# Performance work log

Hardware: AMD Instinct MI355X
Metric: run time of the kernel (lower is better)

The kernel has to match this reference:

```python
import jax, jax.numpy as jnp
import numpy as np

B, C, H, W = 1, 512, 24, 24
N_HEADS, WS = 8, 7
PAD = WS // 2
HEAD_DIM = C // N_HEADS


def setup_inputs() -> dict:
    key = jax.random.key(0)
    ks = jax.random.split(key, 7)
    s = 0.02
    return {
        "x": jax.random.normal(ks[0], (B, C, H, W), dtype=jnp.float32),
        "Wq": s * jax.random.normal(ks[1], (C, C), dtype=jnp.float32),
        "bq": s * jax.random.normal(ks[2], (C,), dtype=jnp.float32),
        "Wk": s * jax.random.normal(ks[3], (C, C), dtype=jnp.float32),
        "bk": s * jax.random.normal(ks[4], (C,), dtype=jnp.float32),
        "Wv": s * jax.random.normal(ks[5], (C, C), dtype=jnp.float32),
        "bv": s * jax.random.normal(ks[6], (C,), dtype=jnp.float32),
        # module initializes gamma to zero; use small nonzero so output depends on attention
        "gamma": jnp.full((1,), 0.1, dtype=jnp.float32),
    }


def _conv1x1(z, Wt, bt):
    # 1x1 Conv2d == per-pixel GEMM over channels
    return jnp.einsum("bchw,oc->bohw", z, Wt) + bt[None, :, None, None]


def _windows(z):
    # z: (B, C, H+ws-1, W+ws-1) -> (B, n_heads, head_dim, ws*ws*H*W)
    # matches torch unfold(2,ws,1).unfold(3,ws,1).permute(0,1,4,5,2,3).view(...)
    taps = [z[:, :, di:di + H, dj:dj + W] for di in range(WS) for dj in range(WS)]
    w = jnp.stack(taps, axis=2)  # (B, C, ws*ws, H, W)
    return w.reshape(B, N_HEADS, HEAD_DIM, WS * WS * H * W)


def reference(x, Wq, bq, Wk, bk, Wv, bv, gamma):
    q = _conv1x1(x, Wq, bq).reshape(B, N_HEADS, HEAD_DIM, H * W)  # (B,h,d,HW)
    xp = jnp.pad(x, ((0, 0), (0, 0), (PAD, PAD), (PAD, PAD)), mode="reflect")
    k = _windows(_conv1x1(xp, Wk, bk))  # (B,h,d,ws^2*HW)
    v = _windows(_conv1x1(xp, Wv, bv))  # (B,h,d,ws^2*HW)
    # NOTE: as written in the source, each query attends to ALL ws^2*H*W keys
    energy = jnp.einsum("bhdq,bhdk->bhqk", q, k)  # (B,h,HW,ws^2*HW)
    attn = jax.nn.softmax(energy, axis=-1)
    out_w = jnp.einsum("bhqk,bhdk->bhdq", attn, v).reshape(B, C, H, W)
    return gamma * out_w + x
```

## Files before the change

### kernel.cpp

```cpp
#include <hip/hip_runtime.h>

#define HW   576
#define CC   512
#define PW   30
#define PPK  1024

typedef float f32x4 __attribute__((ext_vector_type(4)));
typedef short s16x8 __attribute__((ext_vector_type(8)));

__device__ __forceinline__ unsigned short f2bf(float f) {
    unsigned u = __float_as_uint(f);
    return (unsigned short)((u + 0x7FFFu + ((u >> 16) & 1u)) >> 16);
}
__device__ __forceinline__ float bf2f(unsigned short h) {
    return __uint_as_float((unsigned)h << 16);
}
__device__ __forceinline__ int smapf(int p) {
    if (p >= 900) return 576;
    const int y = p / PW, xw = p - y * PW;
    int iy = y - 3;  iy = (iy < 0) ? -iy : (iy > 23 ? 46 - iy : iy);
    int ix = xw - 3; ix = (ix < 0) ? -ix : (ix > 23 ? 46 - ix : ix);
    return iy * 24 + ix;
}

#define OFF_QT 0u
#define OFF_KT 589824u
#define OFF_VP 1638400u
#define OFF_XT 2686976u
#define OFF_WB 3277824u

__global__ __launch_bounds__(256) void cvtT(
    const float* __restrict__ x,
    const float* __restrict__ Wq, const float* __restrict__ Wk,
    const float* __restrict__ Wv,
    unsigned short* __restrict__ xT, unsigned short* __restrict__ wb)
{
    const int b = blockIdx.x, t = threadIdx.x;
    if (b < 72) {
        __shared__ float tile[64][65];
        const int pt = b % 9, ct = b / 9;
        const int p0 = pt * 64, c0 = ct * 64;
        const int tr = t >> 4, tc4 = (t & 15) * 4;
        #pragma unroll
        for (int cr = 0; cr < 4; ++cr) {
            const int row = cr * 16 + tr;
            const float4 v = *(const float4*)&x[(size_t)(c0 + row) * HW + p0 + tc4];
            tile[row][tc4 + 0] = v.x;
            tile[row][tc4 + 1] = v.y;
            tile[row][tc4 + 2] = v.z;
            tile[row][tc4 + 3] = v.w;
        }
        __syncthreads();
        #pragma unroll
        for (int cr = 0; cr < 4; ++cr) {
            const int prow = cr * 16 + tr;
            ushort4 o;
            o.x = f2bf(tile[tc4 + 0][prow]);
            o.y = f2bf(tile[tc4 + 1][prow]);
            o.z = f2bf(tile[tc4 + 2][prow]);
            o.w = f2bf(tile[tc4 + 3][prow]);
            *(ushort4*)&xT[(size_t)(p0 + prow) * CC + c0 + tc4] = o;
        }
    } else if (b == 72) {
        if (t < 128) *(ushort4*)&xT[(size_t)576 * CC + t * 4] = (ushort4){0, 0, 0, 0};
    } else {
        const int wi = (b - 73) * 2048 + t * 8;
        const int sel = wi >> 18, off = wi & 262143;
        const float* src = (sel == 0) ? Wq : (sel == 1) ? Wk : Wv;
        const float4 v0 = *(const float4*)&src[off];
        const float4 v1 = *(const float4*)&src[off + 4];
        ushort4 o0, o1;
        o0.x = f2bf(v0.x); o0.y = f2bf(v0.y); o0.z = f2bf(v0.z); o0.w = f2bf(v0.w);
        o1.x = f2bf(v1.x); o1.y = f2bf(v1.y); o1.z = f2bf(v1.z); o1.w = f2bf(v1.w);
        *(ushort4*)&wb[wi]     = o0;
        *(ushort4*)&wb[wi + 4] = o1;
    }
}

__global__ __launch_bounds__(256) void qkv_direct(
    const unsigned short* __restrict__ xT, const unsigned short* __restrict__ wb,
    const float* __restrict__ bq, const float* __restrict__ bk,
    const float* __restrict__ bv,
    unsigned short* __restrict__ qT, unsigned short* __restrict__ kT,
    unsigned short* __restrict__ vP)
{
    const int t = threadIdx.x;
    const int w = blockIdx.x * 4 + (t >> 6);
    const int lane = t & 63, fr = lane & 15, u = lane >> 4;

    int sel, m0, n0;
    if (w < 576)       { sel = 0; m0 = (w >> 4) << 4;               n0 = (w & 15) << 5; }
    else if (w < 1600) { const int k = w - 576;  sel = 1; m0 = (k >> 4) << 4; n0 = (k & 15) << 5; }
    else               { const int k = w - 1600; sel = 2; m0 = (k >> 5) << 4; n0 = (k & 31) << 5; }

    const unsigned short *A, *B;
    int ar, bn0, bn1;
    if (sel == 0)      { A = xT;          B = wb;          ar = m0 + fr;
                         bn0 = n0 + fr;          bn1 = n0 + 16 + fr; }
    else if (sel == 1) { A = xT;          B = wb + 262144; ar = smapf(m0 + fr);
                         bn0 = n0 + fr;          bn1 = n0 + 16 + fr; }
    else               { A = wb + 524288; B = xT;          ar = m0 + fr;
                         bn0 = smapf(n0 + fr);   bn1 = smapf(n0 + 16 + fr); }

    const unsigned short* Ap  = A + (size_t)ar  * CC + u * 8;
    const unsigned short* Bp0 = B + (size_t)bn0 * CC + u * 8;
    const unsigned short* Bp1 = B + (size_t)bn1 * CC + u * 8;

    f32x4 acc0 = (f32x4){0.f, 0.f, 0.f, 0.f};
    f32x4 acc1 = (f32x4){0.f, 0.f, 0.f, 0.f};
    #pragma unroll 8
    for (int k0 = 0; k0 < CC; k0 += 32) {
        const s16x8 a  = *(const s16x8*)(Ap  + k0);
        const s16x8 b0 = *(const s16x8*)(Bp0 + k0);
        const s16x8 b1 = *(const s16x8*)(Bp1 + k0);
        acc0 = __builtin_amdgcn_mfma_f32_16x16x32_bf16(a, b0, acc0, 0, 0, 0);
        acc1 = __builtin_amdgcn_mfma_f32_16x16x32_bf16(a, b1, acc1, 0, 0, 0);
    }

    #pragma unroll
    for (int ni = 0; ni < 2; ++ni) {
        const f32x4 acc = ni ? acc1 : acc0;
        #pragma unroll
        for (int r = 0; r < 4; ++r) {
            const int m = m0 + u * 4 + r;
            const int n = n0 + ni * 16 + fr;
            if (sel == 0) {
                qT[((size_t)(n >> 6) * HW + m) * 64 + (n & 63)] = f2bf(acc[r] + bq[n]);
            } else if (sel == 1) {
                kT[((size_t)(n >> 6) * PPK + m) * 64 + (n & 63)] = f2bf(acc[r] + bk[n]);
            } else {
                vP[((size_t)(m >> 6) * 64 + (m & 63)) * PPK + n] = f2bf(acc[r] + bv[m]);
            }
        }
    }
}

#define WLS 1040
__global__ __launch_bounds__(256) void attn4(
    const unsigned short* __restrict__ qT, const unsigned short* __restrict__ kT,
    const unsigned short* __restrict__ vP, const float* __restrict__ x,
    const float* __restrict__ gamma, float* __restrict__ out)
{
    const int q0 = blockIdx.x * 16;
    const int hd = blockIdx.y;
    const int t  = threadIdx.x;
    const int lane = t & 63, w = t >> 6;
    const int fr = lane & 15, u = lane >> 4;

    __shared__ float cnt_s[PPK];
    __shared__ __align__(16) unsigned short Wl[16 * WLS];
    __shared__ float mw[64], lw[64], sca[16];

    for (int i = t; i < PPK; i += 256) {
        float c = 0.f;
        if (i < 900) {
            const int y = i / PW, xw = i - y * PW;
            int cy = y + 1;  if (PW - y  < cy) cy = PW - y;  if (cy > 7) cy = 7;
            int cx = xw + 1; if (PW - xw < cx) cx = PW - xw; if (cx > 7) cx = 7;
            c = (float)(cy * cx);
        }
        cnt_s[i] = c;
    }

    const unsigned short* qrow = qT + ((size_t)hd * HW + q0 + fr) * 64 + u * 8;
    const s16x8 b0 = *(const s16x8*)qrow;
    const s16x8 b1 = *(const s16x8*)(qrow + 32);

    f32x4 e[16];
    #pragma unroll
    for (int t4 = 0; t4 < 16; ++t4) {
        const unsigned short* krow =
            kT + ((size_t)hd * PPK + w * 256 + t4 * 16 + fr) * 64 + u * 8;
        const s16x8 a0 = *(const s16x8*)krow;
        const s16x8 a1 = *(const s16x8*)(krow + 32);
        f32x4 a = (f32x4){0.f, 0.f, 0.f, 0.f};
        a = __builtin_amdgcn_mfma_f32_16x16x32_bf16(a0, b0, a, 0, 0, 0);
        a = __builtin_amdgcn_mfma_f32_16x16x32_bf16(a1, b1, a, 0, 0, 0);
        e[t4] = a;
    }

    float m = -1e30f;
    #pragma unroll
    for (int t4 = 0; t4 < 16; ++t4)
        #pragma unroll
        for (int r = 0; r < 4; ++r) m = fmaxf(m, e[t4][r]);
    m = fmaxf(m, __shfl_xor(m, 16));
    m = fmaxf(m, __shfl_xor(m, 32));
    if (lane < 16) mw[w * 16 + lane] = m;
    __syncthreads();
    const float mq = fmaxf(fmaxf(mw[fr], mw[16 + fr]), fmaxf(mw[32 + fr], mw[48 + fr]));

    float sum = 0.f;
    #pragma unroll
    for (int t4 = 0; t4 < 16; ++t4) {
        const float4 c4 = *(const float4*)&cnt_s[w * 256 + t4 * 16 + u * 4];
        const float cw[4] = {c4.x, c4.y, c4.z, c4.w};
        unsigned short wb4[4];
        #pragma unroll
        for (int r = 0; r < 4; ++r) {
            const float wv2 = cw[r] * __expf(e[t4][r] - mq);
            sum += wv2;
            wb4[r] = f2bf(wv2);
        }
        const int ho = fr * WLS + w * 256 + t4 * 16 + u * 4;
        *(unsigned*)&Wl[ho]     = (unsigned)wb4[0] | ((unsigned)wb4[1] << 16);
        *(unsigned*)&Wl[ho + 2] = (unsigned)wb4[2] | ((unsigned)wb4[3] << 16);
    }
    sum += __shfl_xor(sum, 16);
    sum += __shfl_xor(sum, 32);
    if (lane < 16) lw[w * 16 + lane] = sum;
    __syncthreads();

    if (t < 16) {
        const float lq = lw[t] + lw[16 + t] + lw[32 + t] + lw[48 + t];
        sca[t] = gamma[0] / lq;
    }

    f32x4 o = (f32x4){0.f, 0.f, 0.f, 0.f};
    const unsigned short* vrow =
        vP + ((size_t)hd * 64 + w * 16 + fr) * PPK + u * 8;
    #pragma unroll 8
    for (int c = 0; c < 32; ++c) {
        const s16x8 aw = *(const s16x8*)&Wl[fr * WLS + c * 32 + u * 8];
        const s16x8 bv2 = *(const s16x8*)(vrow + c * 32);
        o = __builtin_amdgcn_mfma_f32_16x16x32_bf16(aw, bv2, o, 0, 0, 0);
    }
    __syncthreads();

    const int d = hd * 64 + w * 16 + fr;
    const size_t gb = (size_t)d * HW + q0 + u * 4;
    const float4 x4 = *(const float4*)&x[gb];
    float4 o4;
    o4.x = fmaf(sca[u * 4 + 0], o[0], x4.x);
    o4.y = fmaf(sca[u * 4 + 1], o[1], x4.y);
    o4.z = fmaf(sca[u * 4 + 2], o[2], x4.z);
    o4.w = fmaf(sca[u * 4 + 3], o[3], x4.w);
    *(float4*)&out[gb] = o4;
}

extern "C" void kernel_launch(void* const* d_in, const int* in_sizes, int n_in,
                              void* d_out, int out_size, void* d_ws, size_t ws_size,
                              hipStream_t stream) {
    const float* x     = (const float*)d_in[0];
    const float* Wq    = (const float*)d_in[1];
    const float* bq    = (const float*)d_in[2];
    const float* Wk    = (const float*)d_in[3];
    const float* bk    = (const float*)d_in[4];
    const float* Wv    = (const float*)d_in[5];
    const float* bv    = (const float*)d_in[6];
    const float* gamma = (const float*)d_in[7];
    float* out = (float*)d_out;

    char* wsb = (char*)d_ws;
    unsigned short* qT = (unsigned short*)(wsb + OFF_QT);
    unsigned short* kT = (unsigned short*)(wsb + OFF_KT);
    unsigned short* vP = (unsigned short*)(wsb + OFF_VP);
    unsigned short* xT = (unsigned short*)(wsb + OFF_XT);
    unsigned short* wb = (unsigned short*)(wsb + OFF_WB);

    cvtT<<<dim3(457), 256, 0, stream>>>(x, Wq, Wk, Wv, xT, wb);
    qkv_direct<<<dim3(656), 256, 0, stream>>>(xT, wb, bq, bk, bv, qT, kT, vP);
    attn4<<<dim3(36, 8), 256, 0, stream>>>(qT, kT, vP, x, gamma, out);
}
```

Baseline: 109.0 us.

## Use 32x32 QKV tiles per wave and split attention across 8 waves

The QKV projection kernel now computes a 32x32 output tile per wave with four MFMA accumulators, so each A and B fragment is loaded once and reused twice, halving the wave count. The attention kernel doubles to 512 threads: each wave scores 128 keys instead of 256, and the PV product is split over two key halves whose partial sums are combined through shared memory. This trades fewer redundant global loads and more parallelism for extra reduction steps and synchronisation.

```diff
diff --git a/kernel.cpp b/kernel.cpp
--- a/kernel.cpp
+++ b/kernel.cpp
@@ -89,54 +89,66 @@
     const int lane = t & 63, fr = lane & 15, u = lane >> 4;
 
     int sel, m0, n0;
-    if (w < 576)       { sel = 0; m0 = (w >> 4) << 4;               n0 = (w & 15) << 5; }
-    else if (w < 1600) { const int k = w - 576;  sel = 1; m0 = (k >> 4) << 4; n0 = (k & 15) << 5; }
-    else               { const int k = w - 1600; sel = 2; m0 = (k >> 5) << 4; n0 = (k & 31) << 5; }
+    if (w < 288)      { sel = 0; m0 = (w >> 4) << 5;               n0 = (w & 15) << 5; }
+    else if (w < 800) { const int k = w - 288; sel = 1; m0 = (k >> 4) << 5; n0 = (k & 15) << 5; }
+    else              { const int k = w - 800; sel = 2; m0 = (k >> 5) << 5; n0 = (k & 31) << 5; }
 
     const unsigned short *A, *B;
-    int ar, bn0, bn1;
-    if (sel == 0)      { A = xT;          B = wb;          ar = m0 + fr;
-                         bn0 = n0 + fr;          bn1 = n0 + 16 + fr; }
-    else if (sel == 1) { A = xT;          B = wb + 262144; ar = smapf(m0 + fr);
-                         bn0 = n0 + fr;          bn1 = n0 + 16 + fr; }
-    else               { A = wb + 524288; B = xT;          ar = m0 + fr;
-                         bn0 = smapf(n0 + fr);   bn1 = smapf(n0 + 16 + fr); }
-
-    const unsigned short* Ap  = A + (size_t)ar  * CC + u * 8;
+    int ar0, ar1, bn0, bn1;
+    if (sel == 0)      { A = xT;          B = wb;
+                         ar0 = m0 + fr;         ar1 = m0 + 16 + fr;
+                         bn0 = n0 + fr;         bn1 = n0 + 16 + fr; }
+    else if (sel == 1) { A = xT;          B = wb + 262144;
+                         ar0 = smapf(m0 + fr);  ar1 = smapf(m0 + 16 + fr);
+                         bn0 = n0 + fr;         bn1 = n0 + 16 + fr; }
+    else               { A = wb + 524288; B = xT;
+                         ar0 = m0 + fr;         ar1 = m0 + 16 + fr;
+                         bn0 = smapf(n0 + fr);  bn1 = smapf(n0 + 16 + fr); }
+
+    const unsigned short* Ap0 = A + (size_t)ar0 * CC + u * 8;
+    const unsigned short* Ap1 = A + (size_t)ar1 * CC + u * 8;
     const unsigned short* Bp0 = B + (size_t)bn0 * CC + u * 8;
     const unsigned short* Bp1 = B + (size_t)bn1 * CC + u * 8;
 
-    f32x4 acc0 = (f32x4){0.f, 0.f, 0.f, 0.f};
-    f32x4 acc1 = (f32x4){0.f, 0.f, 0.f, 0.f};
-    #pragma unroll 8
+    f32x4 acc00 = (f32x4){0.f, 0.f, 0.f, 0.f};
+    f32x4 acc01 = (f32x4){0.f, 0.f, 0.f, 0.f};
+    f32x4 acc10 = (f32x4){0.f, 0.f, 0.f, 0.f};
+    f32x4 acc11 = (f32x4){0.f, 0.f, 0.f, 0.f};
+    #pragma unroll 4
     for (int k0 = 0; k0 < CC; k0 += 32) {
-        const s16x8 a  = *(const s16x8*)(Ap  + k0);
+        const s16x8 a0 = *(const s16x8*)(Ap0 + k0);
+        const s16x8 a1 = *(const s16x8*)(Ap1 + k0);
         const s16x8 b0 = *(const s16x8*)(Bp0 + k0);
         const s16x8 b1 = *(const s16x8*)(Bp1 + k0);
-        acc0 = __builtin_amdgcn_mfma_f32_16x16x32_bf16(a, b0, acc0, 0, 0, 0);
-        acc1 = __builtin_amdgcn_mfma_f32_16x16x32_bf16(a, b1, acc1, 0, 0, 0);
-    }
-
-    #pragma unroll
-    for (int ni = 0; ni < 2; ++ni) {
-        const f32x4 acc = ni ? acc1 : acc0;
-        #pragma unroll
-        for (int r = 0; r < 4; ++r) {
-            const int m = m0 + u * 4 + r;
+        acc00 = __builtin_amdgcn_mfma_f32_16x16x32_bf16(a0, b0, acc00, 0, 0, 0);
+        acc01 = __builtin_amdgcn_mfma_f32_16x16x32_bf16(a0, b1, acc01, 0, 0, 0);
+        acc10 = __builtin_amdgcn_mfma_f32_16x16x32_bf16(a1, b0, acc10, 0, 0, 0);
+        acc11 = __builtin_amdgcn_mfma_f32_16x16x32_bf16(a1, b1, acc11, 0, 0, 0);
+    }
+
+    #pragma unroll
+    for (int mi = 0; mi < 2; ++mi) {
+        #pragma unroll
+        for (int ni = 0; ni < 2; ++ni) {
+            const f32x4 acc = mi ? (ni ? acc11 : acc10) : (ni ? acc01 : acc00);
             const int n = n0 + ni * 16 + fr;
-            if (sel == 0) {
-                qT[((size_t)(n >> 6) * HW + m) * 64 + (n & 63)] = f2bf(acc[r] + bq[n]);
-            } else if (sel == 1) {
-                kT[((size_t)(n >> 6) * PPK + m) * 64 + (n & 63)] = f2bf(acc[r] + bk[n]);
-            } else {
-                vP[((size_t)(m >> 6) * 64 + (m & 63)) * PPK + n] = f2bf(acc[r] + bv[m]);
+            #pragma unroll
+            for (int r = 0; r < 4; ++r) {
+                const int m = m0 + mi * 16 + u * 4 + r;
+                if (sel == 0) {
+                    qT[((size_t)(n >> 6) * HW + m) * 64 + (n & 63)] = f2bf(acc[r] + bq[n]);
+                } else if (sel == 1) {
+                    kT[((size_t)(n >> 6) * PPK + m) * 64 + (n & 63)] = f2bf(acc[r] + bk[n]);
+                } else {
+                    vP[((size_t)(m >> 6) * 64 + (m & 63)) * PPK + n] = f2bf(acc[r] + bv[m]);
+                }
             }
         }
     }
 }
 
 #define WLS 1040
-__global__ __launch_bounds__(256) void attn4(
+__global__ __launch_bounds__(512) void attn5(
     const unsigned short* __restrict__ qT, const unsigned short* __restrict__ kT,
     const unsigned short* __restrict__ vP, const float* __restrict__ x,
     const float* __restrict__ gamma, float* __restrict__ out)
@@ -149,9 +161,10 @@
 
     __shared__ float cnt_s[PPK];
     __shared__ __align__(16) unsigned short Wl[16 * WLS];
-    __shared__ float mw[64], lw[64], sca[16];
-
-    for (int i = t; i < PPK; i += 256) {
+    __shared__ float mw[128], lw[128], sca[16];
+    __shared__ float4 red[4][64];
+
+    for (int i = t; i < PPK; i += 512) {
         float c = 0.f;
         if (i < 900) {
             const int y = i / PW, xw = i - y * PW;
@@ -166,11 +179,11 @@
     const s16x8 b0 = *(const s16x8*)qrow;
     const s16x8 b1 = *(const s16x8*)(qrow + 32);
 
-    f32x4 e[16];
-    #pragma unroll
-    for (int t4 = 0; t4 < 16; ++t4) {
+    f32x4 e[8];
+    #pragma unroll
+    for (int t4 = 0; t4 < 8; ++t4) {
         const unsigned short* krow =
-            kT + ((size_t)hd * PPK + w * 256 + t4 * 16 + fr) * 64 + u * 8;
+            kT + ((size_t)hd * PPK + w * 128 + t4 * 16 + fr) * 64 + u * 8;
         const s16x8 a0 = *(const s16x8*)krow;
         const s16x8 a1 = *(const s16x8*)(krow + 32);
         f32x4 a = (f32x4){0.f, 0.f, 0.f, 0.f};
@@ -181,19 +194,21 @@
 
     float m = -1e30f;
     #pragma unroll
-    for (int t4 = 0; t4 < 16; ++t4)
+    for (int t4 = 0; t4 < 8; ++t4)
         #pragma unroll
         for (int r = 0; r < 4; ++r) m = fmaxf(m, e[t4][r]);
     m = fmaxf(m, __shfl_xor(m, 16));
     m = fmaxf(m, __shfl_xor(m, 32));
     if (lane < 16) mw[w * 16 + lane] = m;
     __syncthreads();
-    const float mq = fmaxf(fmaxf(mw[fr], mw[16 + fr]), fmaxf(mw[32 + fr], mw[48 + fr]));
+    float mq = mw[fr];
+    #pragma unroll
+    for (int j = 1; j < 8; ++j) mq = fmaxf(mq, mw[j * 16 + fr]);
 
     float sum = 0.f;
     #pragma unroll
-    for (int t4 = 0; t4 < 16; ++t4) {
-        const float4 c4 = *(const float4*)&cnt_s[w * 256 + t4 * 16 + u * 4];
+    for (int t4 = 0; t4 < 8; ++t4) {
+        const float4 c4 = *(const float4*)&cnt_s[w * 128 + t4 * 16 + u * 4];
         const float cw[4] = {c4.x, c4.y, c4.z, c4.w};
         unsigned short wb4[4];
         #pragma unroll
@@ -202,7 +217,7 @@
             sum += wv2;
             wb4[r] = f2bf(wv2);
         }
-        const int ho = fr * WLS + w * 256 + t4 * 16 + u * 4;
+        const int ho = fr * WLS + w * 128 + t4 * 16 + u * 4;
         *(unsigned*)&Wl[ho]     = (unsigned)wb4[0] | ((unsigned)wb4[1] << 16);
         *(unsigned*)&Wl[ho + 2] = (unsigned)wb4[2] | ((unsigned)wb4[3] << 16);
     }
@@ -212,29 +227,35 @@
     __syncthreads();
 
     if (t < 16) {
-        const float lq = lw[t] + lw[16 + t] + lw[32 + t] + lw[48 + t];
+        float lq = 0.f;
+        #pragma unroll
+        for (int j = 0; j < 8; ++j) lq += lw[j * 16 + t];
         sca[t] = gamma[0] / lq;
     }
 
+    const int dt = w & 3, ph = w >> 2;
     f32x4 o = (f32x4){0.f, 0.f, 0.f, 0.f};
     const unsigned short* vrow =
-        vP + ((size_t)hd * 64 + w * 16 + fr) * PPK + u * 8;
+        vP + ((size_t)hd * 64 + dt * 16 + fr) * PPK + ph * 512 + u * 8;
     #pragma unroll 8
-    for (int c = 0; c < 32; ++c) {
-        const s16x8 aw = *(const s16x8*)&Wl[fr * WLS + c * 32 + u * 8];
+    for (int c = 0; c < 16; ++c) {
+        const s16x8 aw = *(const s16x8*)&Wl[fr * WLS + ph * 512 + c * 32 + u * 8];
         const s16x8 bv2 = *(const s16x8*)(vrow + c * 32);
         o = __builtin_amdgcn_mfma_f32_16x16x32_bf16(aw, bv2, o, 0, 0, 0);
     }
+    if (w >= 4) red[dt][lane] = (float4){o[0], o[1], o[2], o[3]};
     __syncthreads();
-
-    const int d = hd * 64 + w * 16 + fr;
+    if (w >= 4) return;
+
+    const float4 r2 = red[dt][lane];
+    const int d = hd * 64 + dt * 16 + fr;
     const size_t gb = (size_t)d * HW + q0 + u * 4;
     const float4 x4 = *(const float4*)&x[gb];
     float4 o4;
-    o4.x = fmaf(sca[u * 4 + 0], o[0], x4.x);
-    o4.y = fmaf(sca[u * 4 + 1], o[1], x4.y);
-    o4.z = fmaf(sca[u * 4 + 2], o[2], x4.z);
-    o4.w = fmaf(sca[u * 4 + 3], o[3], x4.w);
+    o4.x = fmaf(sca[u * 4 + 0], o[0] + r2.x, x4.x);
+    o4.y = fmaf(sca[u * 4 + 1], o[1] + r2.y, x4.y);
+    o4.z = fmaf(sca[u * 4 + 2], o[2] + r2.z, x4.z);
+    o4.w = fmaf(sca[u * 4 + 3], o[3] + r2.w, x4.w);
     *(float4*)&out[gb] = o4;
 }
 
@@ -259,6 +280,6 @@
     unsigned short* wb = (unsigned short*)(wsb + OFF_WB);
 
     cvtT<<<dim3(457), 256, 0, stream>>>(x, Wq, Wk, Wv, xT, wb);
-    qkv_direct<<<dim3(656), 256, 0, stream>>>(xT, wb, bq, bk, bv, qT, kT, vP);
-    attn4<<<dim3(36, 8), 256, 0, stream>>>(qT, kT, vP, x, gamma, out);
-}
+    qkv_direct<<<dim3(328), 256, 0, stream>>>(xT, wb, bq, bk, bv, qT, kT, vP);
+    attn5<<<dim3(36, 8), 512, 0, stream>>>(qT, kT, vP, x, gamma, out);
+}
```

Result: no change. 107.7 us (-1.2%).
